# Optimization experiments

Hardware: AMD Instinct MI355X
Metric: run time of the kernel (lower is better)

## Reference

```python
import jax, jax.numpy as jnp
import numpy as np

T, B, D, H = 256, 256, 512, 1024


def setup_inputs() -> dict:
    key = jax.random.key(0)
    ks = jax.random.split(key, 9)
    s = 0.02  # small init scale for numerical sanity
    return {
        "inputs": jax.random.normal(ks[0], (T, B, D), dtype=jnp.float32),
        "Wf": jax.random.normal(ks[1], (D + H, H), dtype=jnp.float32) * s,
        "bf": jax.random.normal(ks[2], (H,), dtype=jnp.float32) * s,
        "Wi": jax.random.normal(ks[3], (D + H, H), dtype=jnp.float32) * s,
        "bi": jax.random.normal(ks[4], (H,), dtype=jnp.float32) * s,
        "Wg": jax.random.normal(ks[5], (D + H, H), dtype=jnp.float32) * s,
        "bg": jax.random.normal(ks[6], (H,), dtype=jnp.float32) * s,
        "Wo": jax.random.normal(ks[7], (D + H, H), dtype=jnp.float32) * s,
        "bo": jax.random.normal(ks[8], (H,), dtype=jnp.float32) * s,
    }


def reference(inputs, Wf, bf, Wi, bi, Wg, bg, Wo, bo):
    hidden_dim = Wf.shape[1]
    batch = inputs.shape[1]
    # Fuse the four gate projections into one [D+H, 4H] GEMM per step.
    W = jnp.concatenate([Wf, Wi, Wg, Wo], axis=1)   # [D+H, 4H]
    b = jnp.concatenate([bf, bi, bg, bo], axis=0)   # [4H]

    h0 = jnp.zeros((batch, hidden_dim), dtype=inputs.dtype)
    c0 = jnp.zeros((batch, hidden_dim), dtype=inputs.dtype)

    def step(carry, x):
        hx, cx = carry
        combined = jnp.concatenate([x, hx], axis=1)  # [B, D+H]
        z = combined @ W + b                          # [B, 4H]
        f, i, g, o = jnp.split(z, 4, axis=1)
        f = jax.nn.sigmoid(f)
        i = jax.nn.sigmoid(i)
        g = jnp.tanh(g)
        o = jax.nn.sigmoid(o)
        cx = f * cx + i * g
        hx = o * jnp.tanh(cx)
        return (hx, cx), hx

    (hx, cx), outputs = jax.lax.scan(step, (h0, c0), inputs)
    return outputs, hx, cx
```

## Files before the change

### kernel.cpp

```cpp
#include <hip/hip_runtime.h>
#include <cstdint>
#include <cstddef>

#define T_STEPS 256
#define BATCH   256
#define DIN     512
#define HID     1024
#define KTOT    1536
#define NOUT    4096
#define BHSZ    ((size_t)BATCH * HID)

typedef __bf16 bf16;
typedef __bf16 bf16x4 __attribute__((ext_vector_type(4)));
typedef __bf16 bf16x8 __attribute__((ext_vector_type(8)));
typedef float  f32x4  __attribute__((ext_vector_type(4)));

__device__ __forceinline__ void store_bf16_sc(bf16* p, bf16 v) {
  unsigned short u = __builtin_bit_cast(unsigned short, v);
  asm volatile("global_store_short %0, %1, off sc0 sc1" :: "v"(p), "v"(u) : "memory");
}

#define VMW_(N) asm volatile("s_waitcnt vmcnt(" #N ")" ::: "memory")
#define VMW(N) do { VMW_(N); __builtin_amdgcn_sched_barrier(0); } while (0)
#define SBAR() __builtin_amdgcn_sched_barrier(0)

__device__ __forceinline__ float fexp2(float x) {
  float r; asm("v_exp_f32 %0, %1" : "=v"(r) : "v"(x)); return r;
}
__device__ __forceinline__ float frcp(float x) {
  float r; asm("v_rcp_f32 %0, %1" : "=v"(r) : "v"(x)); return r;
}
__device__ __forceinline__ float fsigmoid(float x) {
  return frcp(1.f + fexp2(-1.44269504f * x));
}
__device__ __forceinline__ float ftanh(float x) {
  return 1.f - 2.f * frcp(1.f + fexp2(2.88539008f * x));
}

__global__ void convert_w_kernel(const float* __restrict__ Wf, const float* __restrict__ Wi,
                                 const float* __restrict__ Wg, const float* __restrict__ Wo,
                                 bf16* __restrict__ Wt) {
  __shared__ float tile[64][17];
  const int k0 = blockIdx.x * 64;
  const int jb = blockIdx.y;
  const int j0 = jb * 16;
  const int t  = threadIdx.x;
  const float* srcs[4] = {Wf, Wi, Wg, Wo};
#pragma unroll
  for (int g = 0; g < 4; ++g) {
    const float* src = srcs[g];
    {
      const int jl = t & 15, kb = t >> 4;
#pragma unroll
      for (int r = 0; r < 4; ++r) {
        const int kl = kb + 16 * r;
        tile[kl][jl] = src[(size_t)(k0 + kl) * HID + (j0 + jl)];
      }
    }
    __syncthreads();
    {
      const int kk = t & 63, jl4 = t >> 6;
#pragma unroll
      for (int r = 0; r < 4; ++r) {
        const int jl = jl4 + 4 * r;
        Wt[(size_t)(jb * 64 + g * 16 + jl) * KTOT + (k0 + kk)] = (bf16)tile[kk][jl];
      }
    }
    __syncthreads();
  }
}

__global__ void convert_x_kernel(const float* __restrict__ X, bf16* __restrict__ xb) {
  const int t = blockIdx.y;
  const int i = blockIdx.x * blockDim.x + threadIdx.x;
  const float4 v = ((const float4*)(X + (size_t)t * BATCH * DIN))[i];
  bf16x4 o;
  o[0] = (bf16)v.x; o[1] = (bf16)v.y; o[2] = (bf16)v.z; o[3] = (bf16)v.w;
  ((bf16x4*)(xb + (size_t)t * BATCH * DIN))[i] = o;
}

__global__ __launch_bounds__(512, 2)
void lstm_v8(const bf16* __restrict__ Bt,
             const bf16* __restrict__ xb,
             bf16* __restrict__ hseq,
             const bf16* __restrict__ zb16,
             float* __restrict__ outF,
             const float* __restrict__ bf_, const float* __restrict__ bi_,
             const float* __restrict__ bg_, const float* __restrict__ bo_,
             unsigned* __restrict__ flags) {
  __shared__ f32x4 redu[8][16][64];

  const int tid = threadIdx.x, lane = tid & 63, wid = tid >> 6;
  const int bid = blockIdx.x;
  const int e8  = bid & 7;
  const int mblk = e8 >> 1;
  const int nblk = ((bid >> 3) << 1) | (e8 & 1);
  const int bm0 = mblk * 64;
  const int bn0 = nblk * 64;
  const int fr = lane & 15, fq = lane >> 4;

  if (tid == 0)
    (void)__hip_atomic_load(flags, __ATOMIC_ACQUIRE, __HIP_MEMORY_SCOPE_AGENT);
  __syncthreads();

  const int j = nblk * 16 + fr;
  const float bfv = bf_[j], biv = bi_[j], bgv = bg_[j], bov = bo_[j];
  float cr[2] = {0.f, 0.f};

  bf16x8 breg[6][4];
#pragma unroll
  for (int s = 0; s < 6; ++s) {
    const int ks = wid + 8 * s;
#pragma unroll
    for (int nf = 0; nf < 4; ++nf)
      breg[s][nf] = *(const bf16x8*)(Bt + (size_t)(bn0 + nf * 16 + fr) * KTOT
                                     + ks * 32 + fq * 8);
  }

  bf16x8 S0[4], S1[4], S2[4], S3[4];

  auto ldx = [&](int t2, int s, bf16x8 (&slot)[4]) {
    const bf16* src = xb + (size_t)t2 * BATCH * DIN + (wid + 8 * s) * 32 + fq * 8;
#pragma unroll
    for (int mf = 0; mf < 4; ++mf)
      slot[mf] = *(const bf16x8*)(src + (size_t)(bm0 + mf * 16 + fr) * DIN);
  };
  auto ldh = [&](int t2, int s, bf16x8 (&slot)[4]) {
    const bf16* base = (t2 == 0) ? zb16 : hseq + (size_t)(t2 - 1) * BHSZ;
    const bf16* src = base + (wid + 8 * s) * 32 - 512 + fq * 8;
#pragma unroll
    for (int mf = 0; mf < 4; ++mf)
      slot[mf] = *(const bf16x8*)(src + (size_t)(bm0 + mf * 16 + fr) * HID);
  };

  auto poll = [&](int tprev) {
    const unsigned* f = flags + (size_t)tprev * 256 + mblk * 64;
    const unsigned long long tt0 = __builtin_amdgcn_s_memrealtime();
    for (;;) {
      unsigned v = __hip_atomic_load(f + lane, __ATOMIC_RELAXED,
                                     __HIP_MEMORY_SCOPE_AGENT);
      if (__all(v != 0)) break;
      __builtin_amdgcn_s_sleep(1);
      if (__builtin_amdgcn_s_memrealtime() - tt0 > (1ULL << 22)) break;
    }
    asm volatile("" ::: "memory");
    __builtin_amdgcn_sched_barrier(0);
  };

#define MFMA16(ACC, SLOT, S) do {                                           \
    __builtin_amdgcn_s_setprio(1);                                          \
    _Pragma("unroll")                                                       \
    for (int mf_ = 0; mf_ < 4; ++mf_) {                                     \
      _Pragma("unroll")                                                     \
      for (int nf_ = 0; nf_ < 4; ++nf_)                                     \
        ACC[mf_][nf_] = __builtin_amdgcn_mfma_f32_16x16x32_bf16(            \
            SLOT[mf_], breg[S][nf_], ACC[mf_][nf_], 0, 0, 0);               \
    }                                                                       \
    __builtin_amdgcn_s_setprio(0);                                          \
  } while (0)

#define STEP(T0, XA, XB, HA, HB, HC, HD, NA, NB) do {                       \
    const int t_ = (T0);                                                    \
    f32x4 acc[4][4] = {};                                                   \
    VMW(4);  MFMA16(acc, XA, 0);                                            \
    VMW(0);  MFMA16(acc, XB, 1);                                            \
    if (t_ > 0) poll(t_ - 1);                    \
    ldh(t_, 2, HA); ldh(t_, 3, HB); ldh(t_, 4, HC); ldh(t_, 5, HD); SBAR(); \
    VMW(12); MFMA16(acc, HA, 2);                                            \
    VMW(8);  MFMA16(acc, HB, 3);                                            \
    VMW(4);  MFMA16(acc, HC, 4);                                            \
    VMW(0);  MFMA16(acc, HD, 5);                                            \
                                  \
    _Pragma("unroll")                                                       \
    for (int mf_ = 0; mf_ < 4; ++mf_) {                                     \
      _Pragma("unroll")                                                     \
      for (int nf_ = 0; nf_ < 4; ++nf_)                                     \
        redu[wid][mf_ * 4 + nf_][lane] = acc[mf_][nf_];                     \
    }                                                                       \
    __syncthreads();                                                        \
    const int fbase_ = (wid >> 1) * 4;                                      \
    const int rh_ = wid & 1;                                                \
    float z_[2][4];                                                         \
    _Pragma("unroll")                                                       \
    for (int e_ = 0; e_ < 2; ++e_) {                                        \
      const int rloc_ = rh_ * 8 + fq * 2 + e_;                              \
      const int lsel_ = (rloc_ >> 2) * 16 + fr;                             \
      const int rc_ = rloc_ & 3;                                            \
      _Pragma("unroll")                                                     \
      for (int nf_ = 0; nf_ < 4; ++nf_) {                                   \
        float sum_ = 0.f;                                                   \
        _Pragma("unroll")                                                   \
        for (int s_ = 0; s_ < 8; ++s_)                                      \
          sum_ += ((const float*)&redu[s_][fbase_ + nf_][lsel_])[rc_];      \
        z_[e_][nf_] = sum_;                                                 \
      }                                                                     \
    }                                                                       \
    float* outSl_ = outF + (size_t)t_ * BHSZ;                               \
    _Pragma("unroll")                                                       \
    for (int e_ = 0; e_ < 2; ++e_) {                                        \
      const float fg_ = fsigmoid(z_[e_][0] + bfv);                          \
      const float ig_ = fsigmoid(z_[e_][1] + biv);                          \
      const float gg_ = ftanh(z_[e_][2] + bgv);                             \
      const float og_ = fsigmoid(z_[e_][3] + bov);                          \
      cr[e_] = fg_ * cr[e_] + ig_ * gg_;                                    \
      const float h_ = og_ * ftanh(cr[e_]);                                 \
      const int m_ = bm0 + wid * 8 + fq * 2 + e_;                           \
      const size_t off_ = (size_t)m_ * HID + j;                             \
      outSl_[off_] = h_;                                                    \
      store_bf16_sc(hseq + (size_t)t_ * BHSZ + off_, (bf16)h_);             \
      if (t_ == T_STEPS - 1)                                                \
        outF[(size_t)(T_STEPS + 1) * BHSZ + off_] = cr[e_];                 \
    }                                                                       \
    if (t_ + 1 < T_STEPS) {                                                 \
      ldx(t_ + 1, 0, NA); ldx(t_ + 1, 1, NB); SBAR();                       \
      VMW(8);              \
    } else {                                                                \
      VMW(0);                                                               \
    }                                                                       \
    __syncthreads();                                                        \
    if (tid == 0)                                                           \
      __hip_atomic_store(&flags[(size_t)t_ * 256 + mblk * 64 + nblk], 1u,   \
                         __ATOMIC_RELAXED, __HIP_MEMORY_SCOPE_AGENT);       \
  } while (0)

  ldx(0, 0, S0); SBAR();
  ldx(0, 1, S1); SBAR();

#pragma unroll 1
  for (int t = 0; t < T_STEPS; t += 2) {
    STEP(t,     S0, S1, S2, S3, S0, S1, S2, S3);
    STEP(t + 1, S2, S3, S0, S1, S2, S3, S0, S1);
  }
#undef STEP
#undef MFMA16
}

__global__ __launch_bounds__(512, 2)
void lstm_fb(const bf16* __restrict__ Bt,
             const float* __restrict__ X,
             const float* __restrict__ zbF,
             float* __restrict__ outF,
             const float* __restrict__ bf_, const float* __restrict__ bi_,
             const float* __restrict__ bg_, const float* __restrict__ bo_,
             unsigned* __restrict__ flags) {
  __shared__ f32x4 redu[8][16][64];
  const int tid = threadIdx.x, lane = tid & 63, wid = tid >> 6;
  const int bid = blockIdx.x;
  const int xcd = bid & 7, sl = bid >> 3;
  const int nblk = xcd * 8 + (sl & 7);
  const int mblk = sl >> 3;
  const int bm0 = mblk * 64;
  const int bn0 = nblk * 64;
  const int fr = lane & 15, fq = lane >> 4;

  if (tid == 0)
    (void)__hip_atomic_load(flags, __ATOMIC_ACQUIRE, __HIP_MEMORY_SCOPE_AGENT);
  __syncthreads();

  const int j = nblk * 16 + fr;
  const float bfv = bf_[j], biv = bi_[j], bgv = bg_[j], bov = bo_[j];
  float cr[2] = {0.f, 0.f};

  bf16x8 breg[6][4];
#pragma unroll
  for (int s = 0; s < 6; ++s) {
    const int ks = wid + 8 * s;
#pragma unroll
    for (int nf = 0; nf < 4; ++nf)
      breg[s][nf] = *(const bf16x8*)(Bt + (size_t)(bn0 + nf * 16 + fr) * KTOT
                                     + ks * 32 + fq * 8);
  }

  bf16x8 afp[2][4];

  auto poll = [&](int tprev) {
    const unsigned* f = flags + (size_t)tprev * 256 + mblk * 64;
    const unsigned long long tt0 = __builtin_amdgcn_s_memrealtime();
    for (;;) {
      unsigned v = __hip_atomic_load(f + lane, __ATOMIC_RELAXED,
                                     __HIP_MEMORY_SCOPE_AGENT);
      if (__all(v != 0)) break;
      __builtin_amdgcn_s_sleep(2);
      if (__builtin_amdgcn_s_memrealtime() - tt0 > (1ULL << 22)) break;
    }
    asm volatile("" ::: "memory");
    __builtin_amdgcn_sched_barrier(0);
  };

  auto loadA = [&](int t2, int s, int p) __attribute__((always_inline)) {
    const int ks = wid + 8 * s;
    const int k = ks * 32 + fq * 8;
    if (s == 2 && t2 > 0) poll(t2 - 1);
    const float* src; int ld, kk;
    if (s < 2) { src = X + (size_t)t2 * BATCH * DIN; ld = DIN; kk = k; }
    else {
      src = (t2 == 0) ? zbF : outF + (size_t)(t2 - 1) * BHSZ;
      ld = HID; kk = k - 512;
    }
#pragma unroll
    for (int mf = 0; mf < 4; ++mf) {
      const float* q = src + (size_t)(bm0 + mf * 16 + fr) * ld + kk;
      const f32x4 lo = *(const f32x4*)q;
      const f32x4 hi = *(const f32x4*)(q + 4);
      bf16x8 v;
      v[0] = (bf16)lo[0]; v[1] = (bf16)lo[1]; v[2] = (bf16)lo[2]; v[3] = (bf16)lo[3];
      v[4] = (bf16)hi[0]; v[5] = (bf16)hi[1]; v[6] = (bf16)hi[2]; v[7] = (bf16)hi[3];
      afp[p][mf] = v;
    }
  };

  loadA(0, 0, 0);

#pragma unroll 1
  for (int t = 0; t < T_STEPS; ++t) {
    f32x4 acc[4][4] = {};
#pragma unroll
    for (int s = 0; s < 6; ++s) {
      if (s < 5)                loadA(t, s + 1, (s + 1) & 1);
      else if (t + 1 < T_STEPS) loadA(t + 1, 0, 0);
      __builtin_amdgcn_s_setprio(1);
#pragma unroll
      for (int mf = 0; mf < 4; ++mf)
#pragma unroll
        for (int nf = 0; nf < 4; ++nf)
          acc[mf][nf] = __builtin_amdgcn_mfma_f32_16x16x32_bf16(
              afp[s & 1][mf], breg[s][nf], acc[mf][nf], 0, 0, 0);
      __builtin_amdgcn_s_setprio(0);
    }

#pragma unroll
    for (int mf = 0; mf < 4; ++mf)
#pragma unroll
      for (int nf = 0; nf < 4; ++nf)
        redu[wid][mf * 4 + nf][lane] = acc[mf][nf];
    __syncthreads();

    const int fbase = (wid >> 1) * 4;
    const int rh = wid & 1;
    float z[2][4];
#pragma unroll
    for (int e = 0; e < 2; ++e) {
      const int rloc = rh * 8 + fq * 2 + e;
      const int lsel = (rloc >> 2) * 16 + fr;
      const int rc = rloc & 3;
#pragma unroll
      for (int nf = 0; nf < 4; ++nf) {
        float sum = 0.f;
#pragma unroll
        for (int s = 0; s < 8; ++s)
          sum += ((const float*)&redu[s][fbase + nf][lsel])[rc];
        z[e][nf] = sum;
      }
    }

    float* outSl = outF + (size_t)t * BHSZ;
#pragma unroll
    for (int e = 0; e < 2; ++e) {
      const float fg = 1.f / (1.f + expf(-(z[e][0] + bfv)));
      const float ig = 1.f / (1.f + expf(-(z[e][1] + biv)));
      const float gg = tanhf(z[e][2] + bgv);
      const float og = 1.f / (1.f + expf(-(z[e][3] + bov)));
      cr[e] = fg * cr[e] + ig * gg;
      const float h = og * tanhf(cr[e]);
      const int m = bm0 + wid * 8 + fq * 2 + e;
      const size_t off = (size_t)m * HID + j;
      __hip_atomic_store(&outSl[off], h, __ATOMIC_RELAXED,
                         __HIP_MEMORY_SCOPE_AGENT);
      if (t == T_STEPS - 1)
        outF[(size_t)(T_STEPS + 1) * BHSZ + off] = cr[e];
    }
    asm volatile("s_waitcnt vmcnt(0)" ::: "memory");
    __syncthreads();
    if (tid == 0)
      __hip_atomic_store(&flags[(size_t)t * 256 + mblk * 64 + nblk], 1u,
                         __ATOMIC_RELAXED, __HIP_MEMORY_SCOPE_AGENT);
  }
}

extern "C" void kernel_launch(void* const* d_in, const int* in_sizes, int n_in,
                              void* d_out, int out_size, void* d_ws, size_t ws_size,
                              hipStream_t stream) {
  const float* X   = (const float*)d_in[0];
  const float* Wf  = (const float*)d_in[1];
  const float* bf_ = (const float*)d_in[2];
  const float* Wi  = (const float*)d_in[3];
  const float* bi_ = (const float*)d_in[4];
  const float* Wg  = (const float*)d_in[5];
  const float* bg_ = (const float*)d_in[6];
  const float* Wo  = (const float*)d_in[7];
  const float* bo_ = (const float*)d_in[8];
  float* out = (float*)d_out;

  const size_t WtB   = (size_t)NOUT * KTOT * 2;
  const size_t zBb   = BHSZ * 4;
  const size_t flagB = (size_t)T_STEPS * 256 * 4;
  const size_t XbB   = (size_t)T_STEPS * BATCH * DIN * 2;
  const size_t HsB   = (size_t)T_STEPS * BHSZ * 2;

  char* ws = (char*)d_ws;
  bf16*     Wt    = (bf16*)ws;              ws += WtB;
  float*    zbF   = (float*)(void*)ws;      ws += zBb;
  unsigned* flags = (unsigned*)(void*)ws;   ws += flagB;

  const bool big = ws_size >= WtB + zBb + flagB + XbB + HsB + (1u << 20);
  bf16* xbp = nullptr;  bf16* hseq = nullptr;
  if (big) {
    xbp  = (bf16*)ws;   ws += XbB;
    hseq = (bf16*)ws;
  }

  hipMemsetAsync(zbF, 0, zBb + flagB, stream);

  convert_w_kernel<<<dim3(KTOT / 64, NOUT / 64), 256, 0, stream>>>(Wf, Wi, Wg, Wo, Wt);

  if (big) {
    convert_x_kernel<<<dim3(BATCH * DIN / 4 / 256, T_STEPS), 256, 0, stream>>>(X, xbp);
    lstm_v8<<<256, 512, 0, stream>>>(Wt, xbp, hseq, (const bf16*)zbF, out,
                                     bf_, bi_, bg_, bo_, flags);
  } else {
    lstm_fb<<<256, 512, 0, stream>>>(Wt, X, zbF, out,
                                     bf_, bi_, bg_, bo_, flags);
  }

  hipMemcpyAsync(out + (size_t)T_STEPS * BHSZ, out + (size_t)(T_STEPS - 1) * BHSZ,
                 BHSZ * 4, hipMemcpyDeviceToDevice, stream);
}
```

Baseline: 2.253 ms.

## Replace per-block barrier+flag with per-wave byte flags and wave-0 relay polling

Each wave now publishes its own completion byte inside a 64-bit per-block flag, so the end-of-step __syncthreads before signalling is removed. Only wave 0 polls the 64 producer flags and relays readiness to the other waves through an LDS variable, which cuts global polling traffic. The loop is also re-peeled so vmcnt waits account for loads still in flight. The risk is extra per-step latency from the LDS relay spin and byte-granular atomics, plus memory-ordering subtleties: each wave's h stores and flag byte are now ordered only by a relaxed store.

```diff
diff --git a/kernel.cpp b/kernel.cpp
--- a/kernel.cpp
+++ b/kernel.cpp
@@ -80,15 +80,16 @@
 }
 
 __global__ __launch_bounds__(512, 2)
-void lstm_v8(const bf16* __restrict__ Bt,
+void lstm_v9(const bf16* __restrict__ Bt,
              const bf16* __restrict__ xb,
              bf16* __restrict__ hseq,
              const bf16* __restrict__ zb16,
              float* __restrict__ outF,
              const float* __restrict__ bf_, const float* __restrict__ bi_,
              const float* __restrict__ bg_, const float* __restrict__ bo_,
-             unsigned* __restrict__ flags) {
+             unsigned long long* __restrict__ flags64) {
   __shared__ f32x4 redu[8][16][64];
+  __shared__ unsigned relay;
 
   const int tid = threadIdx.x, lane = tid & 63, wid = tid >> 6;
   const int bid = blockIdx.x;
@@ -99,8 +100,11 @@
   const int bn0 = nblk * 64;
   const int fr = lane & 15, fq = lane >> 4;
 
-  if (tid == 0)
-    (void)__hip_atomic_load(flags, __ATOMIC_ACQUIRE, __HIP_MEMORY_SCOPE_AGENT);
+  if (tid == 0) {
+    (void)__hip_atomic_load((unsigned*)flags64, __ATOMIC_ACQUIRE,
+                            __HIP_MEMORY_SCOPE_AGENT);
+    relay = 0;
+  }
   __syncthreads();
 
   const int j = nblk * 16 + fr;
@@ -133,13 +137,24 @@
       slot[mf] = *(const bf16x8*)(src + (size_t)(bm0 + mf * 16 + fr) * HID);
   };
 
-  auto poll = [&](int tprev) {
-    const unsigned* f = flags + (size_t)tprev * 256 + mblk * 64;
+  auto pollf = [&](int tprev) {
+    const unsigned long long* f = flags64 + (size_t)tprev * 256 + mblk * 64;
+    const unsigned long long tgt = 0x0101010101010101ULL;
     const unsigned long long tt0 = __builtin_amdgcn_s_memrealtime();
     for (;;) {
-      unsigned v = __hip_atomic_load(f + lane, __ATOMIC_RELAXED,
-                                     __HIP_MEMORY_SCOPE_AGENT);
-      if (__all(v != 0)) break;
+      unsigned long long v = __hip_atomic_load(f + lane, __ATOMIC_RELAXED,
+                                               __HIP_MEMORY_SCOPE_AGENT);
+      if (__all(v == tgt)) break;
+      __builtin_amdgcn_s_sleep(1);
+      if (__builtin_amdgcn_s_memrealtime() - tt0 > (1ULL << 22)) break;
+    }
+    asm volatile("" ::: "memory");
+    __builtin_amdgcn_sched_barrier(0);
+  };
+  auto wait_relay = [&](unsigned tgt) {
+    const unsigned long long tt0 = __builtin_amdgcn_s_memrealtime();
+    while (__hip_atomic_load(&relay, __ATOMIC_ACQUIRE,
+                             __HIP_MEMORY_SCOPE_WORKGROUP) < tgt) {
       __builtin_amdgcn_s_sleep(1);
       if (__builtin_amdgcn_s_memrealtime() - tt0 > (1ULL << 22)) break;
     }
@@ -159,18 +174,27 @@
     __builtin_amdgcn_s_setprio(0);                                          \
   } while (0)
 
-#define STEP(T0, XA, XB, HA, HB, HC, HD, NA, NB) do {                       \
+#define STEP(T0, XA, XB, HA, HB, HC, HD, NA, NB, W0, W1) do {               \
     const int t_ = (T0);                                                    \
     f32x4 acc[4][4] = {};                                                   \
-    VMW(4);  MFMA16(acc, XA, 0);                                            \
-    VMW(0);  MFMA16(acc, XB, 1);                                            \
-    if (t_ > 0) poll(t_ - 1);                    \
+    VMW(W0); MFMA16(acc, XA, 0);                                            \
+    VMW(W1); MFMA16(acc, XB, 1);                                            \
+    if (t_ > 0) {                                                           \
+      if (wid == 0) {                                                       \
+        pollf(t_ - 1);                                                      \
+        if (lane == 0)                                                      \
+          __hip_atomic_store(&relay, (unsigned)t_, __ATOMIC_RELEASE,        \
+                             __HIP_MEMORY_SCOPE_WORKGROUP);                 \
+      } else {                                                              \
+        wait_relay((unsigned)t_);                                           \
+      }                                                                     \
+    }                                                                       \
     ldh(t_, 2, HA); ldh(t_, 3, HB); ldh(t_, 4, HC); ldh(t_, 5, HD); SBAR(); \
     VMW(12); MFMA16(acc, HA, 2);                                            \
     VMW(8);  MFMA16(acc, HB, 3);                                            \
     VMW(4);  MFMA16(acc, HC, 4);                                            \
     VMW(0);  MFMA16(acc, HD, 5);                                            \
-                                  \
+             \
     _Pragma("unroll")                                                       \
     for (int mf_ = 0; mf_ < 4; ++mf_) {                                     \
       _Pragma("unroll")                                                     \
@@ -217,20 +241,24 @@
     } else {                                                                \
       VMW(0);                                                               \
     }                                                                       \
-    __syncthreads();                                                        \
-    if (tid == 0)                                                           \
-      __hip_atomic_store(&flags[(size_t)t_ * 256 + mblk * 64 + nblk], 1u,   \
-                         __ATOMIC_RELAXED, __HIP_MEMORY_SCOPE_AGENT);       \
+    if (lane == 0)                                                          \
+      __hip_atomic_store((unsigned char*)(flags64 + (size_t)t_ * 256        \
+                                          + mblk * 64 + nblk) + wid,        \
+                         (unsigned char)1, __ATOMIC_RELAXED,                \
+                         __HIP_MEMORY_SCOPE_AGENT);                         \
   } while (0)
 
   ldx(0, 0, S0); SBAR();
   ldx(0, 1, S1); SBAR();
 
+  STEP(0, S0, S1, S2, S3, S0, S1, S2, S3, 4, 0);
 #pragma unroll 1
-  for (int t = 0; t < T_STEPS; t += 2) {
-    STEP(t,     S0, S1, S2, S3, S0, S1, S2, S3);
-    STEP(t + 1, S2, S3, S0, S1, S2, S3, S0, S1);
-  }
+  for (int t = 1; t < T_STEPS - 2; t += 2) {
+    STEP(t,     S2, S3, S0, S1, S2, S3, S0, S1, 5, 1);
+    STEP(t + 1, S0, S1, S2, S3, S0, S1, S2, S3, 5, 1);
+  }
+  STEP(T_STEPS - 1, S2, S3, S0, S1, S2, S3, S0, S1, 5, 1);
+
 #undef STEP
 #undef MFMA16
 }
@@ -391,32 +419,34 @@
   const float* bo_ = (const float*)d_in[8];
   float* out = (float*)d_out;
 
-  const size_t WtB   = (size_t)NOUT * KTOT * 2;
-  const size_t zBb   = BHSZ * 4;
-  const size_t flagB = (size_t)T_STEPS * 256 * 4;
-  const size_t XbB   = (size_t)T_STEPS * BATCH * DIN * 2;
-  const size_t HsB   = (size_t)T_STEPS * BHSZ * 2;
+  const size_t WtB    = (size_t)NOUT * KTOT * 2;
+  const size_t zBb    = BHSZ * 4;
+  const size_t fl64B  = (size_t)T_STEPS * 256 * 8;
+  const size_t flagB  = (size_t)T_STEPS * 256 * 4;
+  const size_t XbB    = (size_t)T_STEPS * BATCH * DIN * 2;
+  const size_t HsB    = (size_t)T_STEPS * BHSZ * 2;
 
   char* ws = (char*)d_ws;
-  bf16*     Wt    = (bf16*)ws;              ws += WtB;
-  float*    zbF   = (float*)(void*)ws;      ws += zBb;
-  unsigned* flags = (unsigned*)(void*)ws;   ws += flagB;
-
-  const bool big = ws_size >= WtB + zBb + flagB + XbB + HsB + (1u << 20);
+  bf16*               Wt    = (bf16*)ws;                      ws += WtB;
+  float*              zbF   = (float*)(void*)ws;              ws += zBb;
+  unsigned long long* fl64  = (unsigned long long*)(void*)ws; ws += fl64B;
+  unsigned*           flags = (unsigned*)(void*)ws;           ws += flagB;
+
+  const bool big = ws_size >= WtB + zBb + fl64B + flagB + XbB + HsB + (1u << 20);
   bf16* xbp = nullptr;  bf16* hseq = nullptr;
   if (big) {
     xbp  = (bf16*)ws;   ws += XbB;
     hseq = (bf16*)ws;
   }
 
-  hipMemsetAsync(zbF, 0, zBb + flagB, stream);
+  hipMemsetAsync(zbF, 0, zBb + fl64B + flagB, stream);
 
   convert_w_kernel<<<dim3(KTOT / 64, NOUT / 64), 256, 0, stream>>>(Wf, Wi, Wg, Wo, Wt);
 
   if (big) {
     convert_x_kernel<<<dim3(BATCH * DIN / 4 / 256, T_STEPS), 256, 0, stream>>>(X, xbp);
-    lstm_v8<<<256, 512, 0, stream>>>(Wt, xbp, hseq, (const bf16*)zbF, out,
-                                     bf_, bi_, bg_, bo_, flags);
+    lstm_v9<<<256, 512, 0, stream>>>(Wt, xbp, hseq, (const bf16*)zbF, out,
+                                     bf_, bi_, bg_, bo_, fl64);
   } else {
     lstm_fb<<<256, 512, 0, stream>>>(Wt, X, zbF, out,
                                      bf_, bi_, bg_, bo_, flags);
```

Measured after the change: 3.007 ms. 33.4% more time.
